# Performance work log

Measured on AMD Instinct MI355X. Metric: run time of the kernel, lower is better.

The kernel has to match this reference:

```python
import jax, jax.numpy as jnp
import numpy as np
from jax import lax

N_NODES = 100000
N_EDGES = 1600000
UNITS = 64
DEPTH_EMB = 12
DEPTH_PAR = 5
EPS = 1e-5


def setup_inputs() -> dict:
    key = jax.random.key(0)
    ks = jax.random.split(key, 24)
    x = jax.random.normal(ks[0], (N_NODES, 1), dtype=jnp.float32)
    edge_index = jax.random.randint(ks[1], (2, N_EDGES), 0, N_NODES, dtype=jnp.int32)
    s = 1.0 / np.sqrt(UNITS)
    # GCN conv params: first layer maps feats=1 -> 64, remaining 11 map 64 -> 64
    conv_w0 = jax.random.normal(ks[2], (1, UNITS), dtype=jnp.float32)
    conv_w = jax.random.normal(ks[3], (DEPTH_EMB - 1, UNITS, UNITS), dtype=jnp.float32) * s
    conv_b = jnp.zeros((DEPTH_EMB, UNITS), dtype=jnp.float32)
    # GraphNorm params (applied after every conv except the last)
    gn_gamma = jnp.ones((DEPTH_EMB - 1, UNITS), dtype=jnp.float32)
    gn_beta = jnp.zeros((DEPTH_EMB - 1, UNITS), dtype=jnp.float32)
    gn_alpha = jnp.ones((DEPTH_EMB - 1, UNITS), dtype=jnp.float32)
    # ParNet heads: 4 residual 64->64 linears + final 64->1
    phe_w = jax.random.normal(ks[4], (DEPTH_PAR - 1, UNITS, UNITS), dtype=jnp.float32) * s
    phe_b = jnp.zeros((DEPTH_PAR - 1, UNITS), dtype=jnp.float32)
    phe_wl = jax.random.normal(ks[5], (UNITS, 1), dtype=jnp.float32) * s
    phe_bl = jnp.zeros((1,), dtype=jnp.float32)
    heu_w = jax.random.normal(ks[6], (DEPTH_PAR - 1, UNITS, UNITS), dtype=jnp.float32) * s
    heu_b = jnp.zeros((DEPTH_PAR - 1, UNITS), dtype=jnp.float32)
    heu_wl = jax.random.normal(ks[7], (UNITS, 1), dtype=jnp.float32) * s
    heu_bl = jnp.zeros((1,), dtype=jnp.float32)
    return {"x": x, "edge_index": edge_index,
            "conv_w0": conv_w0, "conv_w": conv_w, "conv_b": conv_b,
            "gn_gamma": gn_gamma, "gn_beta": gn_beta, "gn_alpha": gn_alpha,
            "phe_w": phe_w, "phe_b": phe_b, "phe_wl": phe_wl, "phe_bl": phe_bl,
            "heu_w": heu_w, "heu_b": heu_b, "heu_wl": heu_wl, "heu_bl": heu_bl}


def _graph_norm(h, gamma, beta, alpha):
    # single-graph GraphNorm: per-feature mean over nodes, mean-scale alpha
    mean = jnp.mean(h, axis=0, keepdims=True)            # [1, C]
    hc = h - alpha * mean
    var = jnp.mean(hc * hc, axis=0, keepdims=True)       # [1, C]
    return gamma * hc * lax.rsqrt(var + EPS) + beta


def _parnet(h, ws, bs, wl, bl):
    for i in range(DEPTH_PAR - 1):
        h = jax.nn.relu(h + h @ ws[i] + bs[i])
    return jax.nn.sigmoid(h @ wl + bl)[:, 0]             # [N]


def reference(x, edge_index, conv_w0, conv_w, conv_b, gn_gamma, gn_beta, gn_alpha,
              phe_w, phe_b, phe_wl, phe_bl, heu_w, heu_b, heu_wl, heu_bl):
    n = x.shape[0]
    src, dst = edge_index[0], edge_index[1]
    # GCN symmetric normalization with self-loops
    deg = 1.0 + jax.ops.segment_sum(jnp.ones_like(src, dtype=x.dtype), dst, num_segments=n)
    dinv = lax.rsqrt(deg)                                # [N]
    norm_e = (dinv[src] * dinv[dst])[:, None]            # [E, 1]
    self_norm = (dinv * dinv)[:, None]                   # [N, 1]

    h = x
    for i in range(DEPTH_EMB):
        w = conv_w0 if i == 0 else conv_w[i - 1]
        h = h @ w                                        # [N, 64]
        agg = jax.ops.segment_sum(h[src] * norm_e, dst, num_segments=n)
        h = agg + h * self_norm + conv_b[i]
        if i < DEPTH_EMB - 1:
            h = _graph_norm(h, gn_gamma[i], gn_beta[i], gn_alpha[i])
            h = jax.nn.silu(h)

    phe = _parnet(h, phe_w, phe_b, phe_wl, phe_bl)
    heu = _parnet(h, heu_w, heu_b, heu_wl, heu_bl)
    return (phe, heu)
```

## Files before the change

### kernel.cpp

```cpp
#include <hip/hip_runtime.h>
#include <hip/hip_bf16.h>
#include <hip/hip_fp16.h>
#include <math.h>

#define UNITS 64
#define DEPTH_EMB 12
#define DEPTH_PAR 5
#define GN_EPS 1e-5f


__global__ void k_deg(const int* __restrict__ dst, int* __restrict__ cnt, int E) {
    int e = blockIdx.x * blockDim.x + threadIdx.x;
    if (e < E) atomicAdd(&cnt[dst[e]], 1);
}

__global__ void k_dinv(const int* __restrict__ cnt, float* __restrict__ dinv, int n) {
    int i = blockIdx.x * blockDim.x + threadIdx.x;
    if (i < n) dinv[i] = rsqrtf(1.0f + (float)cnt[i]);
}


__global__ void k_chunksum(const int* __restrict__ cnt, int* __restrict__ csum, int n) {
    __shared__ int sd[256];
    int base = blockIdx.x * 1024;
    int s = 0;
    for (int i = threadIdx.x; i < 1024; i += 256) {
        int idx = base + i;
        if (idx < n) s += cnt[idx];
    }
    sd[threadIdx.x] = s;
    __syncthreads();
    for (int off = 128; off > 0; off >>= 1) {
        if (threadIdx.x < off) sd[threadIdx.x] += sd[threadIdx.x + off];
        __syncthreads();
    }
    if (threadIdx.x == 0) csum[blockIdx.x] = sd[0];
}

__global__ void k_scansum(const int* __restrict__ csum, int* __restrict__ coff,
                          int* __restrict__ rowptr, int nchunks) {
    __shared__ int sd[256];
    int tid = threadIdx.x;
    int v = (tid < nchunks) ? csum[tid] : 0;
    sd[tid] = v;
    __syncthreads();
    for (int off = 1; off < 256; off <<= 1) {
        int t = (tid >= off) ? sd[tid - off] : 0;
        __syncthreads();
        sd[tid] += t;
        __syncthreads();
    }
    if (tid < nchunks) coff[tid] = sd[tid] - v;
    if (tid == 0) rowptr[0] = 0;
}

__global__ void k_scanfinal(const int* __restrict__ cnt, const int* __restrict__ coff,
                            int* __restrict__ rowptr, int n) {
    __shared__ int sd[1024];
    int base = blockIdx.x * 1024;
    int tid = threadIdx.x;
    int idx = base + tid;
    int v = (idx < n) ? cnt[idx] : 0;
    sd[tid] = v;
    __syncthreads();
    for (int off = 1; off < 1024; off <<= 1) {
        int t = (tid >= off) ? sd[tid - off] : 0;
        __syncthreads();
        sd[tid] += t;
        __syncthreads();
    }
    if (idx < n) rowptr[idx + 1] = coff[blockIdx.x] + sd[tid];
}

__global__ void k_fill(const int* __restrict__ src, const int* __restrict__ dst,
                       const int* __restrict__ rowptr, int* __restrict__ fill,
                       int* __restrict__ srcs, int E) {
    int e = blockIdx.x * blockDim.x + threadIdx.x;
    if (e >= E) return;
    int s = src[e], d = dst[e];
    int p = rowptr[d] + atomicAdd(&fill[d], 1);
    srcs[p] = s;
}


__global__ void k_l0(const float* __restrict__ x, const float* __restrict__ w0,
                     const float* __restrict__ dinv, __half* __restrict__ h2, int n) {
    int gid = blockIdx.x * blockDim.x + threadIdx.x;
    if (gid >= n * UNITS) return;
    int node = gid >> 6, c = gid & 63;
    h2[gid] = __float2half(x[node] * w0[c] * dinv[node]);
}

__global__ void k_linear_emb(const float* __restrict__ in, __half* __restrict__ out,
                             const float* __restrict__ W, const float* __restrict__ dinv, int n) {
    int lane = threadIdx.x & 63;
    int wib = threadIdx.x >> 6;
    int wpb = blockDim.x >> 6;
    int gwave = blockIdx.x * wpb + wib;
    int nwaves = gridDim.x * wpb;

    float w[UNITS];
#pragma unroll
    for (int k = 0; k < UNITS; ++k) w[k] = W[k * UNITS + lane];

    for (int nd = gwave; nd < n; nd += nwaves) {
        int node = __builtin_amdgcn_readfirstlane(nd);
        const float* __restrict__ row = in + (size_t)node * UNITS;
        float di = dinv[node];
        float a0 = 0.0f, a1 = 0.0f, a2 = 0.0f, a3 = 0.0f;
#pragma unroll
        for (int k = 0; k < UNITS; k += 4) {
            a0 = fmaf(row[k + 0], w[k + 0], a0);
            a1 = fmaf(row[k + 1], w[k + 1], a1);
            a2 = fmaf(row[k + 2], w[k + 2], a2);
            a3 = fmaf(row[k + 3], w[k + 3], a3);
        }
        float acc = (a0 + a1) + (a2 + a3);
        out[(size_t)node * UNITS + lane] = __float2half(acc * di);
    }
}

__global__ void k_linear_par(const float* __restrict__ in, float* __restrict__ out,
                             const float* __restrict__ W, const float* __restrict__ b, int n) {
    int lane = threadIdx.x & 63;
    int wib = threadIdx.x >> 6;
    int wpb = blockDim.x >> 6;
    int gwave = blockIdx.x * wpb + wib;
    int nwaves = gridDim.x * wpb;

    float w[UNITS];
#pragma unroll
    for (int k = 0; k < UNITS; ++k) w[k] = W[k * UNITS + lane];
    float bj = b[lane];

    for (int nd = gwave; nd < n; nd += nwaves) {
        int node = __builtin_amdgcn_readfirstlane(nd);
        const float* __restrict__ row = in + (size_t)node * UNITS;
        float a0 = 0.0f, a1 = 0.0f, a2 = 0.0f, a3 = 0.0f;
#pragma unroll
        for (int k = 0; k < UNITS; k += 4) {
            a0 = fmaf(row[k + 0], w[k + 0], a0);
            a1 = fmaf(row[k + 1], w[k + 1], a1);
            a2 = fmaf(row[k + 2], w[k + 2], a2);
            a3 = fmaf(row[k + 3], w[k + 3], a3);
        }
        float acc = (a0 + a1) + (a2 + a3) + row[lane] + bj;
        acc = fmaxf(acc, 0.0f);
        out[(size_t)node * UNITS + lane] = acc;
    }
}


template <int DO_STATS>
__global__ void k_gather(const __half* __restrict__ h2, float* __restrict__ h,
                         const int* __restrict__ rowptr, const int* __restrict__ srcs,
                         const float* __restrict__ dinv, const float* __restrict__ b,
                         float* __restrict__ stats, int n) {
    int lane = threadIdx.x & 63;
    int wib = threadIdx.x >> 6;
    int wpb = blockDim.x >> 6;
    int gwave = blockIdx.x * wpb + wib;
    int nwaves = gridDim.x * wpb;
    float bj = b[lane];
    float s1 = 0.0f, s2 = 0.0f;

    for (int nd = gwave; nd < n; nd += nwaves) {
        int node = __builtin_amdgcn_readfirstlane(nd);
        int beg = rowptr[node], end = rowptr[node + 1];
        float di = dinv[node];
        float acc0 = __half2float(h2[(size_t)node * UNITS + lane]);
        float acc1 = 0.0f, acc2 = 0.0f, acc3 = 0.0f;
        int j = beg;
        for (; j + 8 <= end; j += 8) {
            int i0 = srcs[j + 0], i1 = srcs[j + 1], i2 = srcs[j + 2], i3 = srcs[j + 3];
            int i4 = srcs[j + 4], i5 = srcs[j + 5], i6 = srcs[j + 6], i7 = srcs[j + 7];
            float v0 = __half2float(h2[(size_t)i0 * UNITS + lane]);
            float v1 = __half2float(h2[(size_t)i1 * UNITS + lane]);
            float v2 = __half2float(h2[(size_t)i2 * UNITS + lane]);
            float v3 = __half2float(h2[(size_t)i3 * UNITS + lane]);
            float v4 = __half2float(h2[(size_t)i4 * UNITS + lane]);
            float v5 = __half2float(h2[(size_t)i5 * UNITS + lane]);
            float v6 = __half2float(h2[(size_t)i6 * UNITS + lane]);
            float v7 = __half2float(h2[(size_t)i7 * UNITS + lane]);
            acc0 += v0; acc1 += v1; acc2 += v2; acc3 += v3;
            acc0 += v4; acc1 += v5; acc2 += v6; acc3 += v7;
        }
        for (; j + 4 <= end; j += 4) {
            int i0 = srcs[j + 0], i1 = srcs[j + 1], i2 = srcs[j + 2], i3 = srcs[j + 3];
            float v0 = __half2float(h2[(size_t)i0 * UNITS + lane]);
            float v1 = __half2float(h2[(size_t)i1 * UNITS + lane]);
            float v2 = __half2float(h2[(size_t)i2 * UNITS + lane]);
            float v3 = __half2float(h2[(size_t)i3 * UNITS + lane]);
            acc0 += v0; acc1 += v1; acc2 += v2; acc3 += v3;
        }
        for (; j < end; ++j) acc0 += __half2float(h2[(size_t)srcs[j] * UNITS + lane]);
        float acc = (acc0 + acc1) + (acc2 + acc3);
        float hv = fmaf(acc, di, bj);
        h[(size_t)node * UNITS + lane] = hv;
        if (DO_STATS) {
            s1 += hv;
            s2 = fmaf(hv, hv, s2);
        }
    }

    if (DO_STATS) {
        __shared__ float sd[2][4][UNITS];
        sd[0][wib][lane] = s1;
        sd[1][wib][lane] = s2;
        __syncthreads();
        if (threadIdx.x < UNITS) {
            float a1 = 0.0f, a2 = 0.0f;
            for (int r = 0; r < wpb; ++r) {
                a1 += sd[0][r][lane];
                a2 += sd[1][r][lane];
            }
            atomicAdd(&stats[lane], a1);
            atomicAdd(&stats[UNITS + lane], a2);
        }
    }
}


__global__ void k_norm_silu(float4* __restrict__ h, const float* __restrict__ stats,
                            const float* __restrict__ gamma, const float* __restrict__ beta,
                            const float* __restrict__ alpha, float inv_n, int total4) {
    int tid = blockIdx.x * blockDim.x + threadIdx.x;
    int c = (tid & 15) << 2;
    float A[4], Bc[4];
#pragma unroll
    for (int q = 0; q < 4; ++q) {
        float m = stats[c + q] * inv_n;
        float ex2 = stats[UNITS + c + q] * inv_n;
        float a = alpha[c + q];
        float var = ex2 - m * m * (2.0f * a - a * a);
        float g = gamma[c + q] * rsqrtf(var + GN_EPS);
        A[q] = g;
        Bc[q] = beta[c + q] - g * a * m;
    }
    int stride = gridDim.x * blockDim.x;
    for (int gid = tid; gid < total4; gid += stride) {
        float4 v = h[gid];
        float t0 = fmaf(v.x, A[0], Bc[0]);
        float t1 = fmaf(v.y, A[1], Bc[1]);
        float t2 = fmaf(v.z, A[2], Bc[2]);
        float t3 = fmaf(v.w, A[3], Bc[3]);
        v.x = t0 / (1.0f + __expf(-t0));
        v.y = t1 / (1.0f + __expf(-t1));
        v.z = t2 / (1.0f + __expf(-t2));
        v.w = t3 / (1.0f + __expf(-t3));
        h[gid] = v;
    }
}


__global__ void k_head(const float* __restrict__ in, const float* __restrict__ wl,
                       const float* __restrict__ bl, float* __restrict__ out, int n) {
    int lane = threadIdx.x & 63;
    int wib = threadIdx.x >> 6;
    int wpb = blockDim.x >> 6;
    int gwave = blockIdx.x * wpb + wib;
    int nwaves = gridDim.x * wpb;
    float wv = wl[lane];
    float blv = bl[0];
    for (int node = gwave; node < n; node += nwaves) {
        float p = in[(size_t)node * UNITS + lane] * wv;
#pragma unroll
        for (int off = 32; off > 0; off >>= 1) p += __shfl_xor(p, off, 64);
        if (lane == 0) out[node] = 1.0f / (1.0f + __expf(-(p + blv)));
    }
}


extern "C" void kernel_launch(void* const* d_in, const int* in_sizes, int n_in,
                              void* d_out, int out_size, void* d_ws, size_t ws_size,
                              hipStream_t stream) {
    const float* x = (const float*)d_in[0];
    const int* ei = (const int*)d_in[1];
    const float* conv_w0 = (const float*)d_in[2];
    const float* conv_w = (const float*)d_in[3];
    const float* conv_b = (const float*)d_in[4];
    const float* gn_gamma = (const float*)d_in[5];
    const float* gn_beta = (const float*)d_in[6];
    const float* gn_alpha = (const float*)d_in[7];
    const float* phe_w = (const float*)d_in[8];
    const float* phe_b = (const float*)d_in[9];
    const float* phe_wl = (const float*)d_in[10];
    const float* phe_bl = (const float*)d_in[11];
    const float* heu_w = (const float*)d_in[12];
    const float* heu_b = (const float*)d_in[13];
    const float* heu_wl = (const float*)d_in[14];
    const float* heu_bl = (const float*)d_in[15];

    const int N = in_sizes[0];
    const int E = in_sizes[1] / 2;
    const int NC = N * UNITS;
    const int NCHUNK = (N + 1023) / 1024;

    const int* src = ei;
    const int* dstp = ei + E;

    char* w = (char*)d_ws;
    float* dinv = (float*)w;  w += (size_t)N * 4;
    float* h = (float*)w;     w += (size_t)NC * 4;
    float* hx = (float*)w;    w += (size_t)NC * 4;
    float* h3 = (float*)w;    w += (size_t)NC * 4;
    float* stats = (float*)w; w += 128 * 4;
    int* cnt = (int*)w;       w += (size_t)N * 4;
    int* rowptr = (int*)w;    w += (size_t)(N + 1) * 4;
    int* fillc = (int*)w;     w += (size_t)N * 4;
    int* srcs = (int*)w;      w += (size_t)E * 4;
    int* csum = (int*)w;      w += 256 * 4;
    int* coff = (int*)w;      w += 256 * 4;

    __half* h2 = (__half*)hx;
    float* out = (float*)d_out;

    const int B = 256;
    const int gE = (E + B - 1) / B;
    const int gN = (N + B - 1) / B;
    const int gNC = (NC + B - 1) / B;

    hipMemsetAsync(cnt, 0, (size_t)N * 4, stream);
    hipMemsetAsync(fillc, 0, (size_t)N * 4, stream);
    k_deg<<<gE, B, 0, stream>>>(dstp, cnt, E);
    k_dinv<<<gN, B, 0, stream>>>(cnt, dinv, N);
    k_chunksum<<<NCHUNK, 256, 0, stream>>>(cnt, csum, N);
    k_scansum<<<1, 256, 0, stream>>>(csum, coff, rowptr, NCHUNK);
    k_scanfinal<<<NCHUNK, 1024, 0, stream>>>(cnt, coff, rowptr, N);
    k_fill<<<gE, B, 0, stream>>>(src, dstp, rowptr, fillc, srcs, E);

    for (int i = 0; i < DEPTH_EMB; ++i) {
        if (i == 0) {
            k_l0<<<gNC, B, 0, stream>>>(x, conv_w0, dinv, h2, N);
        } else {
            k_linear_emb<<<2048, B, 0, stream>>>(h, h2, conv_w + (size_t)(i - 1) * UNITS * UNITS,
                                                 dinv, N);
        }
        int do_stats = (i < DEPTH_EMB - 1) ? 1 : 0;
        if (do_stats) {
            hipMemsetAsync(stats, 0, 128 * 4, stream);
            k_gather<1><<<2048, B, 0, stream>>>(h2, h, rowptr, srcs, dinv,
                                                conv_b + (size_t)i * UNITS, stats, N);
            k_norm_silu<<<2048, B, 0, stream>>>((float4*)h, stats,
                                                gn_gamma + (size_t)i * UNITS,
                                                gn_beta + (size_t)i * UNITS,
                                                gn_alpha + (size_t)i * UNITS,
                                                1.0f / (float)N, NC / 4);
        } else {
            k_gather<0><<<2048, B, 0, stream>>>(h2, h, rowptr, srcs, dinv,
                                                conv_b + (size_t)i * UNITS, stats, N);
        }
    }

    for (int head = 0; head < 2; ++head) {
        const float* wsrc = head == 0 ? phe_w : heu_w;
        const float* bsrc = head == 0 ? phe_b : heu_b;
        const float* wl = head == 0 ? phe_wl : heu_wl;
        const float* bl = head == 0 ? phe_bl : heu_bl;
        float* o = out + (size_t)head * N;

        const float* cur = h;
        float* nxt = h3;
        for (int l = 0; l < DEPTH_PAR - 1; ++l) {
            k_linear_par<<<2048, B, 0, stream>>>(cur, nxt, wsrc + (size_t)l * UNITS * UNITS,
                                                 bsrc + (size_t)l * UNITS, N);
            cur = nxt;
            nxt = (nxt == h3) ? hx : h3;
        }
        k_head<<<2048, B, 0, stream>>>(cur, wl, bl, o, N);
    }
}
```

Baseline: 1.707 ms.

## Fuse GraphNorm+SiLU into next linear, fuse last ParNet layer with head, deepen gather unroll

Fuses the GraphNorm and SiLU pass into the following embedding linear kernel. Each lane normalises its own feature, and the row is broadcast with wave shuffles instead of being reloaded from memory. The last residual ParNet layer is merged with the sigmoid head, per-layer stats get their own slices with a single upfront memset, and the gather loop gains a 16-wide unrolled stage for more loads in flight. This removes one full read/write pass over the node features per layer and several launches and memsets, at the cost of 64 shuffles per node and higher register pressure.

```diff
diff --git a/kernel.cpp b/kernel.cpp
--- a/kernel.cpp
+++ b/kernel.cpp
@@ -18,7 +18,6 @@
     int i = blockIdx.x * blockDim.x + threadIdx.x;
     if (i < n) dinv[i] = rsqrtf(1.0f + (float)cnt[i]);
 }
-
 
 __global__ void k_chunksum(const int* __restrict__ cnt, int* __restrict__ csum, int n) {
     __shared__ int sd[256];
@@ -89,65 +88,6 @@
     if (gid >= n * UNITS) return;
     int node = gid >> 6, c = gid & 63;
     h2[gid] = __float2half(x[node] * w0[c] * dinv[node]);
-}
-
-__global__ void k_linear_emb(const float* __restrict__ in, __half* __restrict__ out,
-                             const float* __restrict__ W, const float* __restrict__ dinv, int n) {
-    int lane = threadIdx.x & 63;
-    int wib = threadIdx.x >> 6;
-    int wpb = blockDim.x >> 6;
-    int gwave = blockIdx.x * wpb + wib;
-    int nwaves = gridDim.x * wpb;
-
-    float w[UNITS];
-#pragma unroll
-    for (int k = 0; k < UNITS; ++k) w[k] = W[k * UNITS + lane];
-
-    for (int nd = gwave; nd < n; nd += nwaves) {
-        int node = __builtin_amdgcn_readfirstlane(nd);
-        const float* __restrict__ row = in + (size_t)node * UNITS;
-        float di = dinv[node];
-        float a0 = 0.0f, a1 = 0.0f, a2 = 0.0f, a3 = 0.0f;
-#pragma unroll
-        for (int k = 0; k < UNITS; k += 4) {
-            a0 = fmaf(row[k + 0], w[k + 0], a0);
-            a1 = fmaf(row[k + 1], w[k + 1], a1);
-            a2 = fmaf(row[k + 2], w[k + 2], a2);
-            a3 = fmaf(row[k + 3], w[k + 3], a3);
-        }
-        float acc = (a0 + a1) + (a2 + a3);
-        out[(size_t)node * UNITS + lane] = __float2half(acc * di);
-    }
-}
-
-__global__ void k_linear_par(const float* __restrict__ in, float* __restrict__ out,
-                             const float* __restrict__ W, const float* __restrict__ b, int n) {
-    int lane = threadIdx.x & 63;
-    int wib = threadIdx.x >> 6;
-    int wpb = blockDim.x >> 6;
-    int gwave = blockIdx.x * wpb + wib;
-    int nwaves = gridDim.x * wpb;
-
-    float w[UNITS];
-#pragma unroll
-    for (int k = 0; k < UNITS; ++k) w[k] = W[k * UNITS + lane];
-    float bj = b[lane];
-
-    for (int nd = gwave; nd < n; nd += nwaves) {
-        int node = __builtin_amdgcn_readfirstlane(nd);
-        const float* __restrict__ row = in + (size_t)node * UNITS;
-        float a0 = 0.0f, a1 = 0.0f, a2 = 0.0f, a3 = 0.0f;
-#pragma unroll
-        for (int k = 0; k < UNITS; k += 4) {
-            a0 = fmaf(row[k + 0], w[k + 0], a0);
-            a1 = fmaf(row[k + 1], w[k + 1], a1);
-            a2 = fmaf(row[k + 2], w[k + 2], a2);
-            a3 = fmaf(row[k + 3], w[k + 3], a3);
-        }
-        float acc = (a0 + a1) + (a2 + a3) + row[lane] + bj;
-        acc = fmaxf(acc, 0.0f);
-        out[(size_t)node * UNITS + lane] = acc;
-    }
 }
 
 
@@ -171,6 +111,18 @@
         float acc0 = __half2float(h2[(size_t)node * UNITS + lane]);
         float acc1 = 0.0f, acc2 = 0.0f, acc3 = 0.0f;
         int j = beg;
+        for (; j + 16 <= end; j += 16) {
+            int ix[16];
+#pragma unroll
+            for (int q = 0; q < 16; ++q) ix[q] = srcs[j + q];
+            float v[16];
+#pragma unroll
+            for (int q = 0; q < 16; ++q) v[q] = __half2float(h2[(size_t)ix[q] * UNITS + lane]);
+#pragma unroll
+            for (int q = 0; q < 16; q += 4) {
+                acc0 += v[q + 0]; acc1 += v[q + 1]; acc2 += v[q + 2]; acc3 += v[q + 3];
+            }
+        }
         for (; j + 8 <= end; j += 8) {
             int i0 = srcs[j + 0], i1 = srcs[j + 1], i2 = srcs[j + 2], i3 = srcs[j + 3];
             int i4 = srcs[j + 4], i5 = srcs[j + 5], i6 = srcs[j + 6], i7 = srcs[j + 7];
@@ -221,49 +173,110 @@
 }
 
 
-__global__ void k_norm_silu(float4* __restrict__ h, const float* __restrict__ stats,
-                            const float* __restrict__ gamma, const float* __restrict__ beta,
-                            const float* __restrict__ alpha, float inv_n, int total4) {
-    int tid = blockIdx.x * blockDim.x + threadIdx.x;
-    int c = (tid & 15) << 2;
-    float A[4], Bc[4];
-#pragma unroll
-    for (int q = 0; q < 4; ++q) {
-        float m = stats[c + q] * inv_n;
-        float ex2 = stats[UNITS + c + q] * inv_n;
-        float a = alpha[c + q];
-        float var = ex2 - m * m * (2.0f * a - a * a);
-        float g = gamma[c + q] * rsqrtf(var + GN_EPS);
-        A[q] = g;
-        Bc[q] = beta[c + q] - g * a * m;
-    }
-    int stride = gridDim.x * blockDim.x;
-    for (int gid = tid; gid < total4; gid += stride) {
-        float4 v = h[gid];
-        float t0 = fmaf(v.x, A[0], Bc[0]);
-        float t1 = fmaf(v.y, A[1], Bc[1]);
-        float t2 = fmaf(v.z, A[2], Bc[2]);
-        float t3 = fmaf(v.w, A[3], Bc[3]);
-        v.x = t0 / (1.0f + __expf(-t0));
-        v.y = t1 / (1.0f + __expf(-t1));
-        v.z = t2 / (1.0f + __expf(-t2));
-        v.w = t3 / (1.0f + __expf(-t3));
-        h[gid] = v;
-    }
-}
-
-
-__global__ void k_head(const float* __restrict__ in, const float* __restrict__ wl,
-                       const float* __restrict__ bl, float* __restrict__ out, int n) {
+__global__ void k_linear_nsf(const float* __restrict__ in, __half* __restrict__ out,
+                             const float* __restrict__ W, const float* __restrict__ dinv,
+                             const float* __restrict__ stats, const float* __restrict__ gamma,
+                             const float* __restrict__ beta, const float* __restrict__ alpha,
+                             float inv_n, int n) {
     int lane = threadIdx.x & 63;
     int wib = threadIdx.x >> 6;
     int wpb = blockDim.x >> 6;
     int gwave = blockIdx.x * wpb + wib;
     int nwaves = gridDim.x * wpb;
+
+    float w[UNITS];
+#pragma unroll
+    for (int k = 0; k < UNITS; ++k) w[k] = W[k * UNITS + lane];
+
+    float m = stats[lane] * inv_n;
+    float ex2 = stats[UNITS + lane] * inv_n;
+    float al = alpha[lane];
+    float var = ex2 - m * m * (2.0f * al - al * al);
+    float g = gamma[lane] * rsqrtf(var + GN_EPS);
+    float A = g;
+    float Bc = beta[lane] - g * al * m;
+
+    for (int nd = gwave; nd < n; nd += nwaves) {
+        int node = __builtin_amdgcn_readfirstlane(nd);
+        float hv = in[(size_t)node * UNITS + lane];
+        float t = fmaf(hv, A, Bc);
+        t = t / (1.0f + __expf(-t));
+        float di = dinv[node];
+        float a0 = 0.0f, a1 = 0.0f, a2 = 0.0f, a3 = 0.0f;
+#pragma unroll
+        for (int k = 0; k < UNITS; k += 4) {
+            a0 = fmaf(__shfl(t, k + 0, 64), w[k + 0], a0);
+            a1 = fmaf(__shfl(t, k + 1, 64), w[k + 1], a1);
+            a2 = fmaf(__shfl(t, k + 2, 64), w[k + 2], a2);
+            a3 = fmaf(__shfl(t, k + 3, 64), w[k + 3], a3);
+        }
+        float acc = (a0 + a1) + (a2 + a3);
+        out[(size_t)node * UNITS + lane] = __float2half(acc * di);
+    }
+}
+
+
+__global__ void k_linear_par(const float* __restrict__ in, float* __restrict__ out,
+                             const float* __restrict__ W, const float* __restrict__ b, int n) {
+    int lane = threadIdx.x & 63;
+    int wib = threadIdx.x >> 6;
+    int wpb = blockDim.x >> 6;
+    int gwave = blockIdx.x * wpb + wib;
+    int nwaves = gridDim.x * wpb;
+
+    float w[UNITS];
+#pragma unroll
+    for (int k = 0; k < UNITS; ++k) w[k] = W[k * UNITS + lane];
+    float bj = b[lane];
+
+    for (int nd = gwave; nd < n; nd += nwaves) {
+        int node = __builtin_amdgcn_readfirstlane(nd);
+        const float* __restrict__ row = in + (size_t)node * UNITS;
+        float a0 = 0.0f, a1 = 0.0f, a2 = 0.0f, a3 = 0.0f;
+#pragma unroll
+        for (int k = 0; k < UNITS; k += 4) {
+            a0 = fmaf(row[k + 0], w[k + 0], a0);
+            a1 = fmaf(row[k + 1], w[k + 1], a1);
+            a2 = fmaf(row[k + 2], w[k + 2], a2);
+            a3 = fmaf(row[k + 3], w[k + 3], a3);
+        }
+        float acc = (a0 + a1) + (a2 + a3) + row[lane] + bj;
+        acc = fmaxf(acc, 0.0f);
+        out[(size_t)node * UNITS + lane] = acc;
+    }
+}
+
+
+__global__ void k_linear_head(const float* __restrict__ in, const float* __restrict__ W,
+                              const float* __restrict__ b, const float* __restrict__ wl,
+                              const float* __restrict__ bl, float* __restrict__ out, int n) {
+    int lane = threadIdx.x & 63;
+    int wib = threadIdx.x >> 6;
+    int wpb = blockDim.x >> 6;
+    int gwave = blockIdx.x * wpb + wib;
+    int nwaves = gridDim.x * wpb;
+
+    float w[UNITS];
+#pragma unroll
+    for (int k = 0; k < UNITS; ++k) w[k] = W[k * UNITS + lane];
+    float bj = b[lane];
     float wv = wl[lane];
     float blv = bl[0];
-    for (int node = gwave; node < n; node += nwaves) {
-        float p = in[(size_t)node * UNITS + lane] * wv;
+
+    for (int nd = gwave; nd < n; nd += nwaves) {
+        int node = __builtin_amdgcn_readfirstlane(nd);
+        const float* __restrict__ row = in + (size_t)node * UNITS;
+        float a0 = 0.0f, a1 = 0.0f, a2 = 0.0f, a3 = 0.0f;
+#pragma unroll
+        for (int k = 0; k < UNITS; k += 4) {
+            a0 = fmaf(row[k + 0], w[k + 0], a0);
+            a1 = fmaf(row[k + 1], w[k + 1], a1);
+            a2 = fmaf(row[k + 2], w[k + 2], a2);
+            a3 = fmaf(row[k + 3], w[k + 3], a3);
+        }
+        float acc = (a0 + a1) + (a2 + a3) + row[lane] + bj;
+        acc = fmaxf(acc, 0.0f);
+        float p = acc * wv;
 #pragma unroll
         for (int off = 32; off > 0; off >>= 1) p += __shfl_xor(p, off, 64);
         if (lane == 0) out[node] = 1.0f / (1.0f + __expf(-(p + blv)));
@@ -294,7 +307,7 @@
     const int N = in_sizes[0];
     const int E = in_sizes[1] / 2;
     const int NC = N * UNITS;
-    const int NCHUNK = (N + 1023) / 1024;
+    const int NCHUNK1024 = (N + 1023) / 1024;
 
     const int* src = ei;
     const int* dstp = ei + E;
@@ -304,11 +317,11 @@
     float* h = (float*)w;     w += (size_t)NC * 4;
     float* hx = (float*)w;    w += (size_t)NC * 4;
     float* h3 = (float*)w;    w += (size_t)NC * 4;
-    float* stats = (float*)w; w += 128 * 4;
+    float* stats = (float*)w; w += (size_t)DEPTH_EMB * 128 * 4;
     int* cnt = (int*)w;       w += (size_t)N * 4;
     int* rowptr = (int*)w;    w += (size_t)(N + 1) * 4;
     int* fillc = (int*)w;     w += (size_t)N * 4;
-    int* srcs = (int*)w;      w += (size_t)E * 4;
+    int* srcs = (int*)w;      w += (size_t)(E + 16) * 4;
     int* csum = (int*)w;      w += 256 * 4;
     int* coff = (int*)w;      w += 256 * 4;
 
@@ -322,33 +335,29 @@
 
     hipMemsetAsync(cnt, 0, (size_t)N * 4, stream);
     hipMemsetAsync(fillc, 0, (size_t)N * 4, stream);
+    hipMemsetAsync(stats, 0, (size_t)DEPTH_EMB * 128 * 4, stream);
     k_deg<<<gE, B, 0, stream>>>(dstp, cnt, E);
     k_dinv<<<gN, B, 0, stream>>>(cnt, dinv, N);
-    k_chunksum<<<NCHUNK, 256, 0, stream>>>(cnt, csum, N);
-    k_scansum<<<1, 256, 0, stream>>>(csum, coff, rowptr, NCHUNK);
-    k_scanfinal<<<NCHUNK, 1024, 0, stream>>>(cnt, coff, rowptr, N);
+    k_chunksum<<<NCHUNK1024, 256, 0, stream>>>(cnt, csum, N);
+    k_scansum<<<1, 256, 0, stream>>>(csum, coff, rowptr, NCHUNK1024);
+    k_scanfinal<<<NCHUNK1024, 1024, 0, stream>>>(cnt, coff, rowptr, N);
     k_fill<<<gE, B, 0, stream>>>(src, dstp, rowptr, fillc, srcs, E);
 
+    k_l0<<<gNC, B, 0, stream>>>(x, conv_w0, dinv, h2, N);
     for (int i = 0; i < DEPTH_EMB; ++i) {
-        if (i == 0) {
-            k_l0<<<gNC, B, 0, stream>>>(x, conv_w0, dinv, h2, N);
-        } else {
-            k_linear_emb<<<2048, B, 0, stream>>>(h, h2, conv_w + (size_t)(i - 1) * UNITS * UNITS,
-                                                 dinv, N);
-        }
-        int do_stats = (i < DEPTH_EMB - 1) ? 1 : 0;
-        if (do_stats) {
-            hipMemsetAsync(stats, 0, 128 * 4, stream);
+        float* st = stats + (size_t)i * 128;
+        if (i < DEPTH_EMB - 1) {
             k_gather<1><<<2048, B, 0, stream>>>(h2, h, rowptr, srcs, dinv,
-                                                conv_b + (size_t)i * UNITS, stats, N);
-            k_norm_silu<<<2048, B, 0, stream>>>((float4*)h, stats,
-                                                gn_gamma + (size_t)i * UNITS,
-                                                gn_beta + (size_t)i * UNITS,
-                                                gn_alpha + (size_t)i * UNITS,
-                                                1.0f / (float)N, NC / 4);
+                                                conv_b + (size_t)i * UNITS, st, N);
+            k_linear_nsf<<<2048, B, 0, stream>>>(h, h2, conv_w + (size_t)i * UNITS * UNITS,
+                                                 dinv, st,
+                                                 gn_gamma + (size_t)i * UNITS,
+                                                 gn_beta + (size_t)i * UNITS,
+                                                 gn_alpha + (size_t)i * UNITS,
+                                                 1.0f / (float)N, N);
         } else {
             k_gather<0><<<2048, B, 0, stream>>>(h2, h, rowptr, srcs, dinv,
-                                                conv_b + (size_t)i * UNITS, stats, N);
+                                                conv_b + (size_t)i * UNITS, st, N);
         }
     }
 
@@ -359,14 +368,12 @@
         const float* bl = head == 0 ? phe_bl : heu_bl;
         float* o = out + (size_t)head * N;
 
-        const float* cur = h;
-        float* nxt = h3;
-        for (int l = 0; l < DEPTH_PAR - 1; ++l) {
-            k_linear_par<<<2048, B, 0, stream>>>(cur, nxt, wsrc + (size_t)l * UNITS * UNITS,
-                                                 bsrc + (size_t)l * UNITS, N);
-            cur = nxt;
-            nxt = (nxt == h3) ? hx : h3;
-        }
-        k_head<<<2048, B, 0, stream>>>(cur, wl, bl, o, N);
-    }
-}
+        k_linear_par<<<2048, B, 0, stream>>>(h, h3, wsrc, bsrc, N);
+        k_linear_par<<<2048, B, 0, stream>>>(h3, hx, wsrc + (size_t)1 * UNITS * UNITS,
+                                             bsrc + (size_t)1 * UNITS, N);
+        k_linear_par<<<2048, B, 0, stream>>>(hx, h3, wsrc + (size_t)2 * UNITS * UNITS,
+                                             bsrc + (size_t)2 * UNITS, N);
+        k_linear_head<<<2048, B, 0, stream>>>(h3, wsrc + (size_t)3 * UNITS * UNITS,
+                                              bsrc + (size_t)3 * UNITS, wl, bl, o, N);
+    }
+}
```

Measured after the change: 2.059 ms. 1.21x slower.
